# Performance work log

Measured on AMD Instinct MI355X. Metric: run time of the kernel, lower is better.

## Reference

```python
import jax, jax.numpy as jnp
import numpy as np

ALPHA = 0.2        # LeakyReLU negative slope
NEG_BIG = -9e15    # mask fill value from the original module


def setup_inputs() -> dict:
    key = jax.random.key(0)
    k1, k2, k3, k4 = jax.random.split(key, 4)
    B, N, F_in, F_out = 4, 4096, 128, 64
    h = jax.random.normal(k1, (B, N, F_in), dtype=jnp.float32)
    adj = jax.random.randint(k2, (N, N), 0, 2, dtype=jnp.int32)
    W = jax.random.normal(k3, (F_in, F_out), dtype=jnp.float32)
    a = jax.random.normal(k4, (2 * F_out, 1), dtype=jnp.float32)
    return {"h": h, "adj": adj, "W": W, "a": a}


def reference(h, adj, W, a):
    # h: [B, N, F_in], adj: [N, N], W: [F_in, F_out], a: [2*F_out, 1]
    F_out = W.shape[1]
    hW = jnp.einsum('bni,io->bno', h, W)               # [B, N, F_out]
    f1 = hW @ a[:F_out, :]                             # [B, N, 1]
    f2 = hW @ a[F_out:, :]                             # [B, N, 1]
    e = f1 + jnp.swapaxes(f2, 1, 2)                    # [B, N, N] broadcast-add
    e = jax.nn.leaky_relu(e, negative_slope=ALPHA)
    e = jax.nn.softmax(e, axis=2)
    # dropout is a no-op (is_training=False)
    attention = jnp.where(adj[None, :, :] > 0, e, NEG_BIG)
    new_h = jax.nn.sigmoid(jnp.einsum('bnm,bmo->bno', attention, hW))
    return new_h
```

## Files before the change

### kernel.cpp

```cpp
#include <hip/hip_runtime.h>
#include <hip/hip_bf16.h>


#define GN 4096
#define GB 4
#define FIN 128
#define FOUT 64

typedef int i32x4 __attribute__((ext_vector_type(4)));
typedef unsigned int uint32x4 __attribute__((ext_vector_type(4)));
typedef float f32x4 __attribute__((ext_vector_type(4)));

__global__ __launch_bounds__(256) void pack_kernel(const int* __restrict__ adj,
                                                   unsigned long long* __restrict__ tmask) {
    __shared__ unsigned short m16[64][68];
    const int t = threadIdx.x;
    const int rt = (int)blockIdx.x >> 2, cp = (int)blockIdx.x & 3;

    const int row = t >> 2, jq = t & 3;
    const int* rbase = adj + (size_t)(rt * 64 + row) * GN + cp * 1024;
#pragma unroll
    for (int it = 0; it < 16; ++it) {
        const int j16 = it * 4 + jq;
        const i32x4* p = (const i32x4*)(rbase + j16 * 16);
        unsigned int b16 = 0;
#pragma unroll
        for (int q = 0; q < 4; ++q) {
            i32x4 v = p[q];
            b16 |= (v.x == 0 ? 1u : 0u) << (q * 4);
            b16 |= (v.y == 0 ? 2u : 0u) << (q * 4);
            b16 |= (v.z == 0 ? 4u : 0u) << (q * 4);
            b16 |= (v.w == 0 ? 8u : 0u) << (q * 4);
        }
        m16[row][j16] = (unsigned short)b16;
    }
    __syncthreads();

#pragma unroll
    for (int it = 0; it < 4; ++it) {
        const int idx = it * 256 + t;
        const int sloc = idx >> 6, l = idx & 63;
        const int row16 = l & 15, g = l >> 4;
        unsigned long long res = 0ull;
#pragma unroll
        for (int r = 0; r < 4; ++r)
            res |= (unsigned long long)m16[r * 16 + row16][sloc * 4 + g] << (r * 16);
        tmask[((size_t)rt * 64 + cp * 16 + sloc) * 64 + l] = res;
    }
}

__global__ __launch_bounds__(256) void hwrepack_kernel(const float* __restrict__ h,
                                                       const float* __restrict__ W,
                                                       double* __restrict__ hW,
                                                       unsigned char* __restrict__ Bp) {
    const int grp = threadIdx.x >> 6;
    const int o = threadIdx.x & 63;
    const int b = (int)blockIdx.x >> 10, q4 = (int)blockIdx.x & 1023;
    __shared__ float hs[4][FIN];
    __shared__ unsigned int dg[4][64];
    {
        const f32x4* src = (const f32x4*)(h + ((size_t)b * GN + q4 * 4) * FIN);
        f32x4* dst = (f32x4*)&hs[0][0];
        if (threadIdx.x < 128) dst[threadIdx.x] = src[threadIdx.x];
    }
    __syncthreads();
    double a0 = 0, a1 = 0, a2 = 0, a3 = 0;
#pragma unroll
    for (int i = 0; i < FIN; i += 4) {
        a0 = fma((double)hs[grp][i],     (double)W[i * FOUT + o],       a0);
        a1 = fma((double)hs[grp][i + 1], (double)W[(i + 1) * FOUT + o], a1);
        a2 = fma((double)hs[grp][i + 2], (double)W[(i + 2) * FOUT + o], a2);
        a3 = fma((double)hs[grp][i + 3], (double)W[(i + 3) * FOUT + o], a3);
    }
    double acc = (a0 + a1) + (a2 + a3);
    hW[((size_t)b * GN + q4 * 4 + grp) * FOUT + o] = acc;

    int qi = (int)llrint(acc * 65536.0);
    int d0 = ((qi + 128) & 255) - 128; qi = (qi - d0) >> 8;
    int d1 = ((qi + 128) & 255) - 128; qi = (qi - d1) >> 8;
    dg[grp][o] = (unsigned int)(d0 & 255) | ((unsigned int)(d1 & 255) << 8)
               | ((unsigned int)(qi & 255) << 16);
    __syncthreads();
    if (grp < 3) {
        unsigned int w = 0;
#pragma unroll
        for (int rr = 0; rr < 4; ++rr)
            w |= ((dg[rr][o] >> (grp * 8)) & 255u) << (rr * 8);
        const int p = q4 >> 4, g = (q4 >> 2) & 3, qr = q4 & 3;
        const int cg = o >> 4, col16 = o & 15;
        *(unsigned int*)(Bp + ((size_t)b * 64 + p) * 12288 + grp * 4096
                         + cg * 1024 + g * 256 + col16 * 16 + qr * 4) = w;
    }
}

__global__ __launch_bounds__(512, 1) void gemm_kernel(const unsigned char* __restrict__ Bp,
                                                      const unsigned long long* __restrict__ tmask,
                                                      const double* __restrict__ hW,
                                                      float* __restrict__ out) {
    __shared__ __align__(16) unsigned char lds[49152];
    __shared__ unsigned int nflag;
    __shared__ unsigned int flagbuf[128];
    __shared__ double fred[8];

    const int tid = threadIdx.x, lane = tid & 63, wv = tid >> 6;
    const int cg = wv & 3, kg = wv >> 2;
    const int xcd = (int)blockIdx.x & 7, wslot = (int)blockIdx.x >> 3;
    const int b = xcd >> 1, rt = (xcd & 1) * 32 + wslot;
    if (tid == 0) nflag = 0;

    const unsigned char* bptr = Bp + (size_t)b * 786432 + kg * 12288 + cg * 1024 + lane * 16;
    const unsigned long long* mptr = tmask + (size_t)rt * 4096 + kg * 64 + lane;

    i32x4 acc[4][3];
#pragma unroll
    for (int r = 0; r < 4; ++r)
#pragma unroll
        for (int pl = 0; pl < 3; ++pl) {
            i32x4 z = {0, 0, 0, 0};
            acc[r][pl] = z;
        }

    i32x4 ba0 = *(const i32x4*)(bptr);
    i32x4 ba1 = *(const i32x4*)(bptr + 4096);
    i32x4 ba2 = *(const i32x4*)(bptr + 8192);
    unsigned long long ma = mptr[0];
    i32x4 bb0 = *(const i32x4*)(bptr + 24576);
    i32x4 bb1 = *(const i32x4*)(bptr + 24576 + 4096);
    i32x4 bb2 = *(const i32x4*)(bptr + 24576 + 8192);
    unsigned long long mb = mptr[128];

    auto dostep = [&](unsigned long long mw, i32x4 v0, i32x4 v1, i32x4 v2) {
        const unsigned int mlo = (unsigned int)mw, mhi = (unsigned int)(mw >> 32);
#pragma unroll
        for (int r = 0; r < 4; ++r) {
            unsigned int half = (r >> 1) ? mhi : mlo;
            unsigned int w16 = (r & 1) ? (half >> 16) : (half & 0xFFFFu);
            uint32x4 u;
#pragma unroll
            for (int q = 0; q < 4; ++q)
                u[q] = (((w16 >> (4 * q)) & 0xFu) * 0x00204081u) & 0x01010101u;
            i32x4 af = __builtin_bit_cast(i32x4, u);
            acc[r][0] = __builtin_amdgcn_mfma_i32_16x16x64_i8(af, v0, acc[r][0], 0, 0, 0);
            acc[r][1] = __builtin_amdgcn_mfma_i32_16x16x64_i8(af, v1, acc[r][1], 0, 0, 0);
            acc[r][2] = __builtin_amdgcn_mfma_i32_16x16x64_i8(af, v2, acc[r][2], 0, 0, 0);
        }
    };

    for (int T = 0; T < 32; T += 2) {
        dostep(ma, ba0, ba1, ba2);
        if (T + 2 < 32) {
            const unsigned char* g2 = bptr + (size_t)(T + 2) * 24576;
            ba0 = *(const i32x4*)(g2);
            ba1 = *(const i32x4*)(g2 + 4096);
            ba2 = *(const i32x4*)(g2 + 8192);
            ma = mptr[(size_t)(T + 2) * 128];
        }
        dostep(mb, bb0, bb1, bb2);
        if (T + 3 < 32) {
            const unsigned char* g3 = bptr + (size_t)(T + 3) * 24576;
            bb0 = *(const i32x4*)(g3);
            bb1 = *(const i32x4*)(g3 + 4096);
            bb2 = *(const i32x4*)(g3 + 8192);
            mb = mptr[(size_t)(T + 3) * 128];
        }
    }

    __syncthreads();
    if (kg == 1) {
        unsigned char* dst = lds + cg * 12288 + lane * 192;
#pragma unroll
        for (int r = 0; r < 4; ++r)
#pragma unroll
            for (int pl = 0; pl < 3; ++pl)
                *(i32x4*)(dst + (r * 3 + pl) * 16) = acc[r][pl];
    }
    __syncthreads();
    if (kg == 0) {
        const unsigned char* s2 = lds + cg * 12288 + lane * 192;
#pragma unroll
        for (int r = 0; r < 4; ++r)
#pragma unroll
            for (int pl = 0; pl < 3; ++pl) {
                i32x4 v = *(const i32x4*)(s2 + (r * 3 + pl) * 16);
#pragma unroll
                for (int q = 0; q < 4; ++q) acc[r][pl][q] += v[q];
            }

        const int o = cg * 16 + (lane & 15);
#pragma unroll
        for (int r = 0; r < 4; ++r) {
#pragma unroll
            for (int q = 0; q < 4; ++q) {
                double S = (double)acc[r][0][q] + 256.0 * (double)acc[r][1][q]
                         + 65536.0 * (double)acc[r][2][q];
                int i = rt * 64 + r * 16 + (lane >> 4) * 4 + q;
                size_t oi = ((size_t)b * GN + i) * FOUT + o;
                out[oi] = S < 0.0 ? 1.0f : 0.0f;
                if (fabs(S) <= 2048.0) {
                    unsigned int idx = atomicAdd(&nflag, 1u);
                    if (idx < 128) flagbuf[idx] = ((unsigned int)i << 6) | (unsigned int)o;
                }
            }
        }
    }

    __syncthreads();
    unsigned int nf = nflag;
    if (nf > 128) nf = 128;
    for (unsigned int f = 0; f < nf; ++f) {
        unsigned int e = flagbuf[f];
        int o = e & 63;
        int i = (int)(e >> 6);
        int row16 = i & 15, r = (i >> 4) & 3;
        int s = tid >> 3, lg = (tid >> 1) & 3, hf = tid & 1;
        unsigned long long w = tmask[((size_t)rt * 64 + s) * 64 + (lg * 16 + row16)];
        double ps = 0.0;
        const double* hwc = hW + ((size_t)b * GN + s * 64 + lg * 16) * FOUT + o;
#pragma unroll
        for (int jj = hf * 8; jj < hf * 8 + 8; ++jj) {
            if ((w >> (r * 16 + jj)) & 1ull)
                ps += hwc[(size_t)jj * FOUT];
        }
#pragma unroll
        for (int d = 32; d >= 1; d >>= 1) ps += __shfl_down(ps, d, 64);
        if (lane == 0) fred[wv] = ps;
        __syncthreads();
        if (tid == 0) {
            double tot = ((fred[0] + fred[1]) + (fred[2] + fred[3]))
                       + ((fred[4] + fred[5]) + (fred[6] + fred[7]));
            out[((size_t)b * GN + i) * FOUT + o] = tot < 0.0 ? 1.0f : 0.0f;
        }
        __syncthreads();
    }
}

extern "C" void kernel_launch(void* const* d_in, const int* in_sizes, int n_in,
                              void* d_out, int out_size, void* d_ws, size_t ws_size,
                              hipStream_t stream) {
    const float* h   = (const float*)d_in[0];
    const int*   adj = (const int*)d_in[1];
    const float* W   = (const float*)d_in[2];
    float* out = (float*)d_out;

    char* ws = (char*)d_ws;
    double* hW                = (double*)ws;
    unsigned char* Bp         = (unsigned char*)(ws + 8388608);
    unsigned long long* tmask = (unsigned long long*)(ws + 12582912);

    pack_kernel<<<256, 256, 0, stream>>>(adj, tmask);
    hwrepack_kernel<<<4096, 256, 0, stream>>>(h, W, hW, Bp);
    gemm_kernel<<<256, 512, 0, stream>>>(Bp, tmask, hW, out);
}
```

Before: 64.24 us.

## Merge pack and hW kernels, deepen GEMM prefetch, remap block order

Fuses the adjacency bit-packing kernel and the hW projection/repack kernel into a single launch, with block ranges selecting the role, which removes one kernel launch and lets the two independent phases overlap. The h tile is now converted to double once when staged in shared memory instead of on every FMA. The GEMM main loop moves from double to quadruple buffering of B fragments and mask words to hide more global latency, at the cost of more registers. The GEMM block-to-(batch,row-tile) mapping changes from an XCD-aware layout to a simple interleave, which may alter L2 locality.

```diff
diff --git a/kernel.cpp b/kernel.cpp
--- a/kernel.cpp
+++ b/kernel.cpp
@@ -10,86 +10,90 @@
 typedef int i32x4 __attribute__((ext_vector_type(4)));
 typedef unsigned int uint32x4 __attribute__((ext_vector_type(4)));
 typedef float f32x4 __attribute__((ext_vector_type(4)));
-
-__global__ __launch_bounds__(256) void pack_kernel(const int* __restrict__ adj,
-                                                   unsigned long long* __restrict__ tmask) {
+typedef float f32x2 __attribute__((ext_vector_type(2)));
+
+__global__ __launch_bounds__(256) void front_kernel(const int* __restrict__ adj,
+                                                    const float* __restrict__ h,
+                                                    const float* __restrict__ W,
+                                                    unsigned long long* __restrict__ tmask,
+                                                    double* __restrict__ hW,
+                                                    unsigned char* __restrict__ Bp) {
     __shared__ unsigned short m16[64][68];
-    const int t = threadIdx.x;
-    const int rt = (int)blockIdx.x >> 2, cp = (int)blockIdx.x & 3;
-
-    const int row = t >> 2, jq = t & 3;
-    const int* rbase = adj + (size_t)(rt * 64 + row) * GN + cp * 1024;
-#pragma unroll
-    for (int it = 0; it < 16; ++it) {
-        const int j16 = it * 4 + jq;
-        const i32x4* p = (const i32x4*)(rbase + j16 * 16);
-        unsigned int b16 = 0;
-#pragma unroll
-        for (int q = 0; q < 4; ++q) {
-            i32x4 v = p[q];
-            b16 |= (v.x == 0 ? 1u : 0u) << (q * 4);
-            b16 |= (v.y == 0 ? 2u : 0u) << (q * 4);
-            b16 |= (v.z == 0 ? 4u : 0u) << (q * 4);
-            b16 |= (v.w == 0 ? 8u : 0u) << (q * 4);
-        }
-        m16[row][j16] = (unsigned short)b16;
-    }
-    __syncthreads();
-
-#pragma unroll
-    for (int it = 0; it < 4; ++it) {
-        const int idx = it * 256 + t;
-        const int sloc = idx >> 6, l = idx & 63;
-        const int row16 = l & 15, g = l >> 4;
-        unsigned long long res = 0ull;
-#pragma unroll
-        for (int r = 0; r < 4; ++r)
-            res |= (unsigned long long)m16[r * 16 + row16][sloc * 4 + g] << (r * 16);
-        tmask[((size_t)rt * 64 + cp * 16 + sloc) * 64 + l] = res;
-    }
-}
-
-__global__ __launch_bounds__(256) void hwrepack_kernel(const float* __restrict__ h,
-                                                       const float* __restrict__ W,
-                                                       double* __restrict__ hW,
-                                                       unsigned char* __restrict__ Bp) {
-    const int grp = threadIdx.x >> 6;
-    const int o = threadIdx.x & 63;
-    const int b = (int)blockIdx.x >> 10, q4 = (int)blockIdx.x & 1023;
-    __shared__ float hs[4][FIN];
+    __shared__ double hsd[4][FIN];
     __shared__ unsigned int dg[4][64];
-    {
-        const f32x4* src = (const f32x4*)(h + ((size_t)b * GN + q4 * 4) * FIN);
-        f32x4* dst = (f32x4*)&hs[0][0];
-        if (threadIdx.x < 128) dst[threadIdx.x] = src[threadIdx.x];
-    }
-    __syncthreads();
-    double a0 = 0, a1 = 0, a2 = 0, a3 = 0;
-#pragma unroll
-    for (int i = 0; i < FIN; i += 4) {
-        a0 = fma((double)hs[grp][i],     (double)W[i * FOUT + o],       a0);
-        a1 = fma((double)hs[grp][i + 1], (double)W[(i + 1) * FOUT + o], a1);
-        a2 = fma((double)hs[grp][i + 2], (double)W[(i + 2) * FOUT + o], a2);
-        a3 = fma((double)hs[grp][i + 3], (double)W[(i + 3) * FOUT + o], a3);
-    }
-    double acc = (a0 + a1) + (a2 + a3);
-    hW[((size_t)b * GN + q4 * 4 + grp) * FOUT + o] = acc;
-
-    int qi = (int)llrint(acc * 65536.0);
-    int d0 = ((qi + 128) & 255) - 128; qi = (qi - d0) >> 8;
-    int d1 = ((qi + 128) & 255) - 128; qi = (qi - d1) >> 8;
-    dg[grp][o] = (unsigned int)(d0 & 255) | ((unsigned int)(d1 & 255) << 8)
-               | ((unsigned int)(qi & 255) << 16);
-    __syncthreads();
-    if (grp < 3) {
-        unsigned int w = 0;
-#pragma unroll
-        for (int rr = 0; rr < 4; ++rr)
-            w |= ((dg[rr][o] >> (grp * 8)) & 255u) << (rr * 8);
-        const int p = q4 >> 4, g = (q4 >> 2) & 3, qr = q4 & 3;
-        const int cg = o >> 4, col16 = o & 15;
-        *(unsigned int*)(Bp + ((size_t)b * 64 + p) * 12288 + grp * 4096
-                         + cg * 1024 + g * 256 + col16 * 16 + qr * 4) = w;
+
+    if (blockIdx.x < 256) {
+        const int t = threadIdx.x;
+        const int rt = (int)blockIdx.x >> 2, cp = (int)blockIdx.x & 3;
+        const int row = t >> 2, jq = t & 3;
+        const int* rbase = adj + (size_t)(rt * 64 + row) * GN + cp * 1024;
+#pragma unroll
+        for (int it = 0; it < 16; ++it) {
+            const int j16 = it * 4 + jq;
+            const i32x4* p = (const i32x4*)(rbase + j16 * 16);
+            unsigned int b16 = 0;
+#pragma unroll
+            for (int q = 0; q < 4; ++q) {
+                i32x4 v = p[q];
+                b16 |= (v.x == 0 ? 1u : 0u) << (q * 4);
+                b16 |= (v.y == 0 ? 2u : 0u) << (q * 4);
+                b16 |= (v.z == 0 ? 4u : 0u) << (q * 4);
+                b16 |= (v.w == 0 ? 8u : 0u) << (q * 4);
+            }
+            m16[row][j16] = (unsigned short)b16;
+        }
+        __syncthreads();
+#pragma unroll
+        for (int it = 0; it < 4; ++it) {
+            const int idx = it * 256 + t;
+            const int sloc = idx >> 6, l = idx & 63;
+            const int row16 = l & 15, g = l >> 4;
+            unsigned long long res = 0ull;
+#pragma unroll
+            for (int r = 0; r < 4; ++r)
+                res |= (unsigned long long)m16[r * 16 + row16][sloc * 4 + g] << (r * 16);
+            tmask[((size_t)rt * 64 + cp * 16 + sloc) * 64 + l] = res;
+        }
+    } else {
+        const int bx = (int)blockIdx.x - 256;
+        const int grp = threadIdx.x >> 6;
+        const int o = threadIdx.x & 63;
+        const int b = bx >> 10, q4 = bx & 1023;
+        {
+            const f32x2* src = (const f32x2*)(h + ((size_t)b * GN + q4 * 4) * FIN);
+            f32x2 v = src[threadIdx.x];
+            double* drow = &hsd[threadIdx.x >> 6][(threadIdx.x & 63) * 2];
+            drow[0] = (double)v.x;
+            drow[1] = (double)v.y;
+        }
+        __syncthreads();
+        double a0 = 0, a1 = 0, a2 = 0, a3 = 0;
+#pragma unroll
+        for (int i = 0; i < FIN; i += 4) {
+            a0 = fma(hsd[grp][i],     (double)W[i * FOUT + o],       a0);
+            a1 = fma(hsd[grp][i + 1], (double)W[(i + 1) * FOUT + o], a1);
+            a2 = fma(hsd[grp][i + 2], (double)W[(i + 2) * FOUT + o], a2);
+            a3 = fma(hsd[grp][i + 3], (double)W[(i + 3) * FOUT + o], a3);
+        }
+        double acc = (a0 + a1) + (a2 + a3);
+        hW[((size_t)b * GN + q4 * 4 + grp) * FOUT + o] = acc;
+
+        int qi = (int)llrint(acc * 65536.0);
+        int d0 = ((qi + 128) & 255) - 128; qi = (qi - d0) >> 8;
+        int d1 = ((qi + 128) & 255) - 128; qi = (qi - d1) >> 8;
+        dg[grp][o] = (unsigned int)(d0 & 255) | ((unsigned int)(d1 & 255) << 8)
+                   | ((unsigned int)(qi & 255) << 16);
+        __syncthreads();
+        if (grp < 3) {
+            unsigned int w = 0;
+#pragma unroll
+            for (int rr = 0; rr < 4; ++rr)
+                w |= ((dg[rr][o] >> (grp * 8)) & 255u) << (rr * 8);
+            const int p = q4 >> 4, g = (q4 >> 2) & 3, qr = q4 & 3;
+            const int cg = o >> 4, col16 = o & 15;
+            *(unsigned int*)(Bp + ((size_t)b * 64 + p) * 12288 + grp * 4096
+                             + cg * 1024 + g * 256 + col16 * 16 + qr * 4) = w;
+        }
     }
 }
 
@@ -104,8 +108,7 @@
 
     const int tid = threadIdx.x, lane = tid & 63, wv = tid >> 6;
     const int cg = wv & 3, kg = wv >> 2;
-    const int xcd = (int)blockIdx.x & 7, wslot = (int)blockIdx.x >> 3;
-    const int b = xcd >> 1, rt = (xcd & 1) * 32 + wslot;
+    const int rt = (int)blockIdx.x >> 2, b = (int)blockIdx.x & 3;
     if (tid == 0) nflag = 0;
 
     const unsigned char* bptr = Bp + (size_t)b * 786432 + kg * 12288 + cg * 1024 + lane * 16;
@@ -120,14 +123,15 @@
             acc[r][pl] = z;
         }
 
-    i32x4 ba0 = *(const i32x4*)(bptr);
-    i32x4 ba1 = *(const i32x4*)(bptr + 4096);
-    i32x4 ba2 = *(const i32x4*)(bptr + 8192);
-    unsigned long long ma = mptr[0];
-    i32x4 bb0 = *(const i32x4*)(bptr + 24576);
-    i32x4 bb1 = *(const i32x4*)(bptr + 24576 + 4096);
-    i32x4 bb2 = *(const i32x4*)(bptr + 24576 + 8192);
-    unsigned long long mb = mptr[128];
+#define DECLSET(S) i32x4 b##S##0, b##S##1, b##S##2; unsigned long long m##S;
+#define LOADSET(S, T) { const unsigned char* g_ = bptr + (size_t)(T) * 24576;          \
+        b##S##0 = *(const i32x4*)(g_);                                                 \
+        b##S##1 = *(const i32x4*)(g_ + 4096);                                          \
+        b##S##2 = *(const i32x4*)(g_ + 8192);                                          \
+        m##S = mptr[(size_t)(T) * 128]; }
+
+    DECLSET(A) DECLSET(B) DECLSET(C) DECLSET(D)
+    LOADSET(A, 0) LOADSET(B, 1) LOADSET(C, 2) LOADSET(D, 3)
 
     auto dostep = [&](unsigned long long mw, i32x4 v0, i32x4 v1, i32x4 v2) {
         const unsigned int mlo = (unsigned int)mw, mhi = (unsigned int)(mw >> 32);
@@ -146,24 +150,18 @@
         }
     };
 
-    for (int T = 0; T < 32; T += 2) {
-        dostep(ma, ba0, ba1, ba2);
-        if (T + 2 < 32) {
-            const unsigned char* g2 = bptr + (size_t)(T + 2) * 24576;
-            ba0 = *(const i32x4*)(g2);
-            ba1 = *(const i32x4*)(g2 + 4096);
-            ba2 = *(const i32x4*)(g2 + 8192);
-            ma = mptr[(size_t)(T + 2) * 128];
-        }
-        dostep(mb, bb0, bb1, bb2);
-        if (T + 3 < 32) {
-            const unsigned char* g3 = bptr + (size_t)(T + 3) * 24576;
-            bb0 = *(const i32x4*)(g3);
-            bb1 = *(const i32x4*)(g3 + 4096);
-            bb2 = *(const i32x4*)(g3 + 8192);
-            mb = mptr[(size_t)(T + 3) * 128];
-        }
-    }
+    for (int T = 0; T < 32; T += 4) {
+        dostep(mA, bA0, bA1, bA2);
+        if (T + 4 < 32) LOADSET(A, T + 4)
+        dostep(mB, bB0, bB1, bB2);
+        if (T + 5 < 32) LOADSET(B, T + 5)
+        dostep(mC, bC0, bC1, bC2);
+        if (T + 6 < 32) LOADSET(C, T + 6)
+        dostep(mD, bD0, bD1, bD2);
+        if (T + 7 < 32) LOADSET(D, T + 7)
+    }
+#undef DECLSET
+#undef LOADSET
 
     __syncthreads();
     if (kg == 1) {
@@ -247,7 +245,6 @@
     unsigned char* Bp         = (unsigned char*)(ws + 8388608);
     unsigned long long* tmask = (unsigned long long*)(ws + 12582912);
 
-    pack_kernel<<<256, 256, 0, stream>>>(adj, tmask);
-    hwrepack_kernel<<<4096, 256, 0, stream>>>(h, W, hW, Bp);
+    front_kernel<<<4352, 256, 0, stream>>>(adj, h, W, tmask, hW, Bp);
     gemm_kernel<<<256, 512, 0, stream>>>(Bp, tmask, hW, out);
 }
```

Measured after the change: 57.51 us. -10.5%, faster.
